# Optimization experiments

Hardware: AMD Instinct MI355X
Metric: run time of the kernel (lower is better)

Reference implementation:

```python
import jax, jax.numpy as jnp
import numpy as np
import math

B, NB, HID, KD, NH = 256, 16, 512, 64, 8

def setup_inputs() -> dict:
    key = jax.random.key(0)
    ks = jax.random.split(key, 6)
    s = lambda fan_in: 1.0 / math.sqrt(fan_in)
    return {
        "h": jax.random.normal(ks[0], (B, NB, HID), dtype=jnp.float32),
        "mask": jax.random.randint(ks[1], (B, NB), 0, 2, dtype=jnp.int32),
        "Wk": jax.random.normal(ks[2], (NB, HID, KD * NH), dtype=jnp.float32) * s(HID),
        "Wq": jax.random.normal(ks[3], (NB, HID, KD * NH), dtype=jnp.float32) * s(HID),
        "Wv": jax.random.normal(ks[4], (NB, HID, HID * NH), dtype=jnp.float32) * s(HID),
        "Wo": jax.random.normal(ks[5], (NB, HID * NH, HID), dtype=jnp.float32) * s(HID * NH),
    }

def _group_linear(x, w):
    # x: (B, NB, din), w: (NB, din, dout) -> (B, NB, dout)
    return jnp.einsum('bnd,nde->bne', x, w)

def reference(h, mask, Wk, Wq, Wv, Wo):
    # grouped QKV projections
    k = _group_linear(h, Wk).reshape(B, NB, NH, KD).transpose(0, 2, 1, 3)    # (B,H,NB,KD)
    q = _group_linear(h, Wq).reshape(B, NB, NH, KD).transpose(0, 2, 1, 3)    # (B,H,NB,KD)
    v = _group_linear(h, Wv).reshape(B, NB, NH, HID).transpose(0, 2, 1, 3)   # (B,H,NB,HID)
    scores = jnp.einsum('bhqd,bhkd->bhqk', q, k) / math.sqrt(KD)             # (B,H,NB,NB)
    probs = jax.nn.softmax(scores, axis=-1)
    # post-softmax row mask: mask (B,NB) -> (B,1,NB,1)
    probs = probs * mask.astype(probs.dtype)[:, None, :, None]
    ctx = jnp.einsum('bhqk,bhkd->bhqd', probs, v)                            # (B,H,NB,HID)
    ctx = ctx.transpose(0, 2, 1, 3).reshape(B, NB, NH * HID)                 # (B,NB,H*HID)
    return _group_linear(ctx, Wo)                                            # (B,NB,HID)
```

## Files before the change

kernel.cpp:

```cpp
#include <hip/hip_runtime.h>


typedef short s16x4 __attribute__((ext_vector_type(4)));
typedef short s16x8 __attribute__((ext_vector_type(8)));
typedef float f32x4 __attribute__((ext_vector_type(4)));

__device__ __forceinline__ unsigned short f2bf(float f) {
  unsigned int u = __builtin_bit_cast(unsigned int, f);
  u += 0x7fffu + ((u >> 16) & 1u);
  return (unsigned short)(u >> 16);
}
__device__ __forceinline__ float bf2f(unsigned short s) {
  unsigned int u = ((unsigned int)s) << 16;
  return __builtin_bit_cast(float, u);
}

__global__ __launch_bounds__(256) void cvt_h(const float* __restrict__ h,
                                             unsigned short* __restrict__ hb)
{
  int i = (blockIdx.x * 256 + threadIdx.x) * 4;
  float4 v = *reinterpret_cast<const float4*>(h + i);
  s16x4 st = { (short)f2bf(v.x), (short)f2bf(v.y), (short)f2bf(v.z), (short)f2bf(v.w) };
  *reinterpret_cast<s16x4*>(hb + i) = st;
}

__global__ __launch_bounds__(512) void qkv_gemm(
    const unsigned short* __restrict__ hb, const float* __restrict__ Wq,
    const float* __restrict__ Wk, const float* __restrict__ Wv,
    unsigned short* __restrict__ qo, unsigned short* __restrict__ ko,
    unsigned short* __restrict__ vo)
{
  const int g    = blockIdx.y;
  const int n0   = blockIdx.x * 64;
  const int tid  = threadIdx.x;
  const int lane = tid & 63;
  const int wave = tid >> 6;
  const int wm   = (wave >> 1) * 64;
  const int wn   = (wave & 1) * 32;

  const float* W; unsigned short* out; size_t obase; int oldc, wN, c0;
  if (n0 < 512)       { W = Wq + (size_t)g * 262144;  out = qo; obase = (size_t)g * 512;  oldc = 8192;  wN = 512;  c0 = n0; }
  else if (n0 < 1024) { W = Wk + (size_t)g * 262144;  out = ko; obase = (size_t)g * 512;  oldc = 8192;  wN = 512;  c0 = n0 - 512; }
  else                { W = Wv + (size_t)g * 2097152; out = vo; obase = (size_t)g * 4096; oldc = 65536; wN = 4096; c0 = n0 - 1024; }

  const unsigned short* A = hb + (size_t)g * 512;

  __shared__ unsigned short As[256][40];
  __shared__ unsigned short Bs[64][36];

  f32x4 acc[4][2];
  #pragma unroll
  for (int i = 0; i < 4; i++)
    #pragma unroll
    for (int j = 0; j < 2; j++) acc[i][j] = (f32x4){0.f, 0.f, 0.f, 0.f};

  const int fr = lane & 15, fq = lane >> 4;
  const int arow = tid >> 2, akq = tid & 3;
  const int bn = tid & 63, bkc = tid >> 6;

  s16x8 aR0[2], aR1[2];
  f32x4 bR0, bR1;

  auto LOAD0 = [&](int k0) {
    #pragma unroll
    for (int p = 0; p < 2; p++)
      aR0[p] = *reinterpret_cast<const s16x8*>(A + (size_t)(p * 128 + arow) * 8192 + k0 + akq * 8);
    const float* wp = W + (size_t)(k0 + bkc * 4) * wN + c0 + bn;
    bR0 = (f32x4){ wp[0], wp[wN], wp[2 * wN], wp[3 * wN] };
  };
  auto LOAD1 = [&](int k0) {
    #pragma unroll
    for (int p = 0; p < 2; p++)
      aR1[p] = *reinterpret_cast<const s16x8*>(A + (size_t)(p * 128 + arow) * 8192 + k0 + akq * 8);
    const float* wp = W + (size_t)(k0 + bkc * 4) * wN + c0 + bn;
    bR1 = (f32x4){ wp[0], wp[wN], wp[2 * wN], wp[3 * wN] };
  };
  auto STORE0 = [&]() {
    #pragma unroll
    for (int p = 0; p < 2; p++)
      *reinterpret_cast<s16x8*>(&As[p * 128 + arow][akq * 8]) = aR0[p];
    s16x4 st = { (short)f2bf(bR0[0]), (short)f2bf(bR0[1]),
                 (short)f2bf(bR0[2]), (short)f2bf(bR0[3]) };
    *reinterpret_cast<s16x4*>(&Bs[bn][bkc * 4]) = st;
  };
  auto STORE1 = [&]() {
    #pragma unroll
    for (int p = 0; p < 2; p++)
      *reinterpret_cast<s16x8*>(&As[p * 128 + arow][akq * 8]) = aR1[p];
    s16x4 st = { (short)f2bf(bR1[0]), (short)f2bf(bR1[1]),
                 (short)f2bf(bR1[2]), (short)f2bf(bR1[3]) };
    *reinterpret_cast<s16x4*>(&Bs[bn][bkc * 4]) = st;
  };
  auto COMPUTE = [&]() {
    s16x8 af[4], bfr[2];
    #pragma unroll
    for (int mi = 0; mi < 4; mi++)
      af[mi] = *reinterpret_cast<const s16x8*>(&As[wm + mi * 16 + fr][fq * 8]);
    #pragma unroll
    for (int ni = 0; ni < 2; ni++) {
      const s16x4* bp = reinterpret_cast<const s16x4*>(&Bs[wn + ni * 16 + fr][fq * 8]);
      s16x4 lo = bp[0], hi = bp[1];
      bfr[ni] = __builtin_shufflevector(lo, hi, 0, 1, 2, 3, 4, 5, 6, 7);
    }
    #pragma unroll
    for (int mi = 0; mi < 4; mi++)
      #pragma unroll
      for (int ni = 0; ni < 2; ni++)
        acc[mi][ni] = __builtin_amdgcn_mfma_f32_16x16x32_bf16(af[mi], bfr[ni], acc[mi][ni], 0, 0, 0);
  };

  LOAD0(0);
  LOAD1(32);
  STORE0();
  __syncthreads();

  for (int k0 = 0; k0 < 512; k0 += 64) {
    if (k0 + 64 < 512) LOAD0(k0 + 64);
    COMPUTE();
    __syncthreads();
    STORE1();
    __syncthreads();
    if (k0 + 96 < 512) LOAD1(k0 + 96);
    COMPUTE();
    if (k0 + 64 < 512) {
      __syncthreads();
      STORE0();
      __syncthreads();
    }
  }

  #pragma unroll
  for (int mi = 0; mi < 4; mi++)
    #pragma unroll
    for (int ni = 0; ni < 2; ni++)
      #pragma unroll
      for (int r = 0; r < 4; r++) {
        int row = wm + mi * 16 + fq * 4 + r;
        int col = c0 + wn + ni * 16 + fr;
        out[obase + (size_t)row * oldc + col] = f2bf(acc[mi][ni][r]);
      }
}

__global__ __launch_bounds__(256) void attn_kernel(
    const unsigned short* __restrict__ q, const unsigned short* __restrict__ k,
    const unsigned short* __restrict__ v, const int* __restrict__ mask,
    unsigned short* __restrict__ ctx)
{
  const int b  = blockIdx.x >> 3;
  const int hh = blockIdx.x & 7;
  const int tid = threadIdx.x;

  __shared__ float qs[16][65];
  __shared__ float ks[16][65];
  __shared__ float sc[16][16];

  {
    int n = tid >> 4, d4 = (tid & 15) * 4;
    size_t gi = ((size_t)(b * 16 + n) << 9) + (hh << 6) + d4;
    ushort4 qv = *reinterpret_cast<const ushort4*>(q + gi);
    ushort4 kv = *reinterpret_cast<const ushort4*>(k + gi);
    qs[n][d4] = bf2f(qv.x); qs[n][d4+1] = bf2f(qv.y); qs[n][d4+2] = bf2f(qv.z); qs[n][d4+3] = bf2f(qv.w);
    ks[n][d4] = bf2f(kv.x); ks[n][d4+1] = bf2f(kv.y); ks[n][d4+2] = bf2f(kv.z); ks[n][d4+3] = bf2f(kv.w);
  }
  __syncthreads();
  {
    int qi = tid >> 4, ki = tid & 15;
    float s = 0.f;
    #pragma unroll
    for (int j = 0; j < 64; j++) s += qs[qi][j] * ks[ki][j];
    sc[qi][ki] = s * 0.125f;
  }
  __syncthreads();
  if (tid < 16) {
    float m = sc[tid][0];
    #pragma unroll
    for (int j = 1; j < 16; j++) m = fmaxf(m, sc[tid][j]);
    float ev[16], sum = 0.f;
    #pragma unroll
    for (int j = 0; j < 16; j++) { ev[j] = __expf(sc[tid][j] - m); sum += ev[j]; }
    float scale = (mask[b * 16 + tid] != 0) ? (1.f / sum) : 0.f;
    #pragma unroll
    for (int j = 0; j < 16; j++) sc[tid][j] = ev[j] * scale;
  }
  __syncthreads();
  {
    int col4  = (tid & 127) * 4;
    int qbase = (tid >> 7) * 8;
    float a0[8], a1[8], a2[8], a3[8];
    #pragma unroll
    for (int j = 0; j < 8; j++) { a0[j] = 0.f; a1[j] = 0.f; a2[j] = 0.f; a3[j] = 0.f; }
    #pragma unroll
    for (int kk = 0; kk < 16; kk++) {
      ushort4 vv = *reinterpret_cast<const ushort4*>(
          v + ((size_t)(b * 16 + kk) << 12) + (hh << 9) + col4);
      float v0 = bf2f(vv.x), v1 = bf2f(vv.y), v2 = bf2f(vv.z), v3 = bf2f(vv.w);
      #pragma unroll
      for (int j = 0; j < 8; j++) {
        float p = sc[qbase + j][kk];
        a0[j] += p * v0; a1[j] += p * v1; a2[j] += p * v2; a3[j] += p * v3;
      }
    }
    #pragma unroll
    for (int j = 0; j < 8; j++) {
      ushort4 st = { f2bf(a0[j]), f2bf(a1[j]), f2bf(a2[j]), f2bf(a3[j]) };
      *reinterpret_cast<ushort4*>(
          ctx + ((size_t)(b * 16 + qbase + j) << 12) + (hh << 9) + col4) = st;
    }
  }
}

__global__ __launch_bounds__(512) void out_gemm(
    const unsigned short* __restrict__ ctxp, const float* __restrict__ Wo,
    float* __restrict__ partial)
{
  const int g    = blockIdx.y;
  const int bx   = blockIdx.x;
  const int sk   = bx >> 3;
  const int n0   = (bx & 7) * 64;
  const int tid  = threadIdx.x;
  const int lane = tid & 63;
  const int wave = tid >> 6;
  const int wm   = (wave >> 1) * 64;
  const int wn   = (wave & 1) * 32;

  const unsigned short* A = ctxp + (size_t)g * 4096;
  const float* W = Wo + (size_t)g * 2097152;

  __shared__ unsigned short As[256][40];
  __shared__ unsigned short Bs[64][36];

  f32x4 acc[4][2];
  #pragma unroll
  for (int i = 0; i < 4; i++)
    #pragma unroll
    for (int j = 0; j < 2; j++) acc[i][j] = (f32x4){0.f, 0.f, 0.f, 0.f};

  const int fr = lane & 15, fq = lane >> 4;
  const int arow = tid >> 2, akq = tid & 3;
  const int bn = tid & 63, bkc = tid >> 6;

  s16x8 aR0[2], aR1[2];
  f32x4 bR0, bR1;

  auto LOAD0 = [&](int k0) {
    #pragma unroll
    for (int p = 0; p < 2; p++)
      aR0[p] = *reinterpret_cast<const s16x8*>(A + (size_t)(p * 128 + arow) * 65536 + k0 + akq * 8);
    const float* wp = W + (size_t)(k0 + bkc * 4) * 512 + n0 + bn;
    bR0 = (f32x4){ wp[0], wp[512], wp[1024], wp[1536] };
  };
  auto LOAD1 = [&](int k0) {
    #pragma unroll
    for (int p = 0; p < 2; p++)
      aR1[p] = *reinterpret_cast<const s16x8*>(A + (size_t)(p * 128 + arow) * 65536 + k0 + akq * 8);
    const float* wp = W + (size_t)(k0 + bkc * 4) * 512 + n0 + bn;
    bR1 = (f32x4){ wp[0], wp[512], wp[1024], wp[1536] };
  };
  auto STORE0 = [&]() {
    #pragma unroll
    for (int p = 0; p < 2; p++)
      *reinterpret_cast<s16x8*>(&As[p * 128 + arow][akq * 8]) = aR0[p];
    s16x4 st = { (short)f2bf(bR0[0]), (short)f2bf(bR0[1]),
                 (short)f2bf(bR0[2]), (short)f2bf(bR0[3]) };
    *reinterpret_cast<s16x4*>(&Bs[bn][bkc * 4]) = st;
  };
  auto STORE1 = [&]() {
    #pragma unroll
    for (int p = 0; p < 2; p++)
      *reinterpret_cast<s16x8*>(&As[p * 128 + arow][akq * 8]) = aR1[p];
    s16x4 st = { (short)f2bf(bR1[0]), (short)f2bf(bR1[1]),
                 (short)f2bf(bR1[2]), (short)f2bf(bR1[3]) };
    *reinterpret_cast<s16x4*>(&Bs[bn][bkc * 4]) = st;
  };
  auto COMPUTE = [&]() {
    s16x8 af[4], bfr[2];
    #pragma unroll
    for (int mi = 0; mi < 4; mi++)
      af[mi] = *reinterpret_cast<const s16x8*>(&As[wm + mi * 16 + fr][fq * 8]);
    #pragma unroll
    for (int ni = 0; ni < 2; ni++) {
      const s16x4* bp = reinterpret_cast<const s16x4*>(&Bs[wn + ni * 16 + fr][fq * 8]);
      s16x4 lo = bp[0], hi = bp[1];
      bfr[ni] = __builtin_shufflevector(lo, hi, 0, 1, 2, 3, 4, 5, 6, 7);
    }
    #pragma unroll
    for (int mi = 0; mi < 4; mi++)
      #pragma unroll
      for (int ni = 0; ni < 2; ni++)
        acc[mi][ni] = __builtin_amdgcn_mfma_f32_16x16x32_bf16(af[mi], bfr[ni], acc[mi][ni], 0, 0, 0);
  };

  const int ks = sk * 1024, kend = ks + 1024;

  LOAD0(ks);
  LOAD1(ks + 32);
  STORE0();
  __syncthreads();

  for (int k0 = ks; k0 < kend; k0 += 64) {
    if (k0 + 64 < kend) LOAD0(k0 + 64);
    COMPUTE();
    __syncthreads();
    STORE1();
    __syncthreads();
    if (k0 + 96 < kend) LOAD1(k0 + 96);
    COMPUTE();
    if (k0 + 64 < kend) {
      __syncthreads();
      STORE0();
      __syncthreads();
    }
  }

  float* pg = partial + (size_t)sk * 2097152 + (size_t)g * 512;
  #pragma unroll
  for (int mi = 0; mi < 4; mi++)
    #pragma unroll
    for (int ni = 0; ni < 2; ni++)
      #pragma unroll
      for (int r = 0; r < 4; r++) {
        int row = wm + mi * 16 + fq * 4 + r;
        int col = n0 + wn + ni * 16 + fr;
        pg[(size_t)row * 8192 + col] = acc[mi][ni][r];
      }
}

__global__ __launch_bounds__(256) void reduce4(const float* __restrict__ part,
                                               float* __restrict__ out)
{
  int i = (blockIdx.x * 256 + threadIdx.x) * 4;
  float4 a = *reinterpret_cast<const float4*>(part + i);
  float4 b = *reinterpret_cast<const float4*>(part + 2097152 + i);
  float4 c = *reinterpret_cast<const float4*>(part + 4194304 + i);
  float4 d = *reinterpret_cast<const float4*>(part + 6291456 + i);
  float4 s = { a.x + b.x + c.x + d.x, a.y + b.y + c.y + d.y,
               a.z + b.z + c.z + d.z, a.w + b.w + c.w + d.w };
  *reinterpret_cast<float4*>(out + i) = s;
}

extern "C" void kernel_launch(void* const* d_in, const int* in_sizes, int n_in,
                              void* d_out, int out_size, void* d_ws, size_t ws_size,
                              hipStream_t stream) {
  const float* h  = (const float*)d_in[0];
  const int* mask = (const int*)d_in[1];
  const float* Wk = (const float*)d_in[2];
  const float* Wq = (const float*)d_in[3];
  const float* Wv = (const float*)d_in[4];
  const float* Wo = (const float*)d_in[5];
  float* out = (float*)d_out;

  unsigned short* qws   = (unsigned short*)d_ws;
  unsigned short* kws   = qws + 2097152;
  unsigned short* vws   = kws + 2097152;
  unsigned short* ctxws = vws + 16777216;
  unsigned short* hb    = ctxws;
  float* part           = (float*)d_ws;

  cvt_h<<<2048, 256, 0, stream>>>(h, hb);
  qkv_gemm<<<dim3(80, 16), 512, 0, stream>>>(hb, Wq, Wk, Wv, qws, kws, vws);
  attn_kernel<<<2048, 256, 0, stream>>>(qws, kws, vws, mask, ctxws);
  out_gemm<<<dim3(32, 16), 512, 0, stream>>>(ctxws, Wo, part);
  reduce4<<<2048, 256, 0, stream>>>(part, out);
}
```

Before: 389.8 us.

## Double-buffer LDS tiles in GEMMs to halve barriers per k-step

Both the QKV and output GEMMs now keep two LDS buffers, one per half-step, so each store goes to the buffer not being read. This removes one of the two block barriers around each store. The plain __syncthreads is replaced by an explicit lgkmcnt wait plus s_barrier, and the B-weight global loads are issued before the A loads. LDS use per block doubles, which may lower occupancy. The lighter barrier may not order the global loads the way __syncthreads did.

```diff
diff --git a/kernel.cpp b/kernel.cpp
--- a/kernel.cpp
+++ b/kernel.cpp
@@ -13,6 +13,11 @@
 __device__ __forceinline__ float bf2f(unsigned short s) {
   unsigned int u = ((unsigned int)s) << 16;
   return __builtin_bit_cast(float, u);
+}
+
+__device__ __forceinline__ void lds_barrier() {
+  asm volatile("s_waitcnt lgkmcnt(0)" ::: "memory");
+  __builtin_amdgcn_s_barrier();
 }
 
 __global__ __launch_bounds__(256) void cvt_h(const float* __restrict__ h,
@@ -45,8 +50,8 @@
 
   const unsigned short* A = hb + (size_t)g * 512;
 
-  __shared__ unsigned short As[256][40];
-  __shared__ unsigned short Bs[64][36];
+  __shared__ unsigned short As[2][256][40];
+  __shared__ unsigned short Bs[2][64][36];
 
   f32x4 acc[4][2];
   #pragma unroll
@@ -62,43 +67,43 @@
   f32x4 bR0, bR1;
 
   auto LOAD0 = [&](int k0) {
-    #pragma unroll
-    for (int p = 0; p < 2; p++)
-      aR0[p] = *reinterpret_cast<const s16x8*>(A + (size_t)(p * 128 + arow) * 8192 + k0 + akq * 8);
     const float* wp = W + (size_t)(k0 + bkc * 4) * wN + c0 + bn;
     bR0 = (f32x4){ wp[0], wp[wN], wp[2 * wN], wp[3 * wN] };
+    #pragma unroll
+    for (int p = 0; p < 2; p++)
+      aR0[p] = *reinterpret_cast<const s16x8*>(A + (size_t)(p * 128 + arow) * 8192 + k0 + akq * 8);
   };
   auto LOAD1 = [&](int k0) {
-    #pragma unroll
-    for (int p = 0; p < 2; p++)
-      aR1[p] = *reinterpret_cast<const s16x8*>(A + (size_t)(p * 128 + arow) * 8192 + k0 + akq * 8);
     const float* wp = W + (size_t)(k0 + bkc * 4) * wN + c0 + bn;
     bR1 = (f32x4){ wp[0], wp[wN], wp[2 * wN], wp[3 * wN] };
+    #pragma unroll
+    for (int p = 0; p < 2; p++)
+      aR1[p] = *reinterpret_cast<const s16x8*>(A + (size_t)(p * 128 + arow) * 8192 + k0 + akq * 8);
   };
   auto STORE0 = [&]() {
     #pragma unroll
     for (int p = 0; p < 2; p++)
-      *reinterpret_cast<s16x8*>(&As[p * 128 + arow][akq * 8]) = aR0[p];
+      *reinterpret_cast<s16x8*>(&As[0][p * 128 + arow][akq * 8]) = aR0[p];
     s16x4 st = { (short)f2bf(bR0[0]), (short)f2bf(bR0[1]),
                  (short)f2bf(bR0[2]), (short)f2bf(bR0[3]) };
-    *reinterpret_cast<s16x4*>(&Bs[bn][bkc * 4]) = st;
+    *reinterpret_cast<s16x4*>(&Bs[0][bn][bkc * 4]) = st;
   };
   auto STORE1 = [&]() {
     #pragma unroll
     for (int p = 0; p < 2; p++)
-      *reinterpret_cast<s16x8*>(&As[p * 128 + arow][akq * 8]) = aR1[p];
+      *reinterpret_cast<s16x8*>(&As[1][p * 128 + arow][akq * 8]) = aR1[p];
     s16x4 st = { (short)f2bf(bR1[0]), (short)f2bf(bR1[1]),
                  (short)f2bf(bR1[2]), (short)f2bf(bR1[3]) };
-    *reinterpret_cast<s16x4*>(&Bs[bn][bkc * 4]) = st;
-  };
-  auto COMPUTE = [&]() {
+    *reinterpret_cast<s16x4*>(&Bs[1][bn][bkc * 4]) = st;
+  };
+  auto COMPUTE = [&](int buf) {
     s16x8 af[4], bfr[2];
     #pragma unroll
     for (int mi = 0; mi < 4; mi++)
-      af[mi] = *reinterpret_cast<const s16x8*>(&As[wm + mi * 16 + fr][fq * 8]);
+      af[mi] = *reinterpret_cast<const s16x8*>(&As[buf][wm + mi * 16 + fr][fq * 8]);
     #pragma unroll
     for (int ni = 0; ni < 2; ni++) {
-      const s16x4* bp = reinterpret_cast<const s16x4*>(&Bs[wn + ni * 16 + fr][fq * 8]);
+      const s16x4* bp = reinterpret_cast<const s16x4*>(&Bs[buf][wn + ni * 16 + fr][fq * 8]);
       s16x4 lo = bp[0], hi = bp[1];
       bfr[ni] = __builtin_shufflevector(lo, hi, 0, 1, 2, 3, 4, 5, 6, 7);
     }
@@ -112,20 +117,18 @@
   LOAD0(0);
   LOAD1(32);
   STORE0();
-  __syncthreads();
+  lds_barrier();
 
   for (int k0 = 0; k0 < 512; k0 += 64) {
     if (k0 + 64 < 512) LOAD0(k0 + 64);
-    COMPUTE();
-    __syncthreads();
+    COMPUTE(0);
     STORE1();
-    __syncthreads();
+    lds_barrier();
     if (k0 + 96 < 512) LOAD1(k0 + 96);
-    COMPUTE();
+    COMPUTE(1);
     if (k0 + 64 < 512) {
-      __syncthreads();
       STORE0();
-      __syncthreads();
+      lds_barrier();
     }
   }
 
@@ -226,8 +229,8 @@
   const unsigned short* A = ctxp + (size_t)g * 4096;
   const float* W = Wo + (size_t)g * 2097152;
 
-  __shared__ unsigned short As[256][40];
-  __shared__ unsigned short Bs[64][36];
+  __shared__ unsigned short As[2][256][40];
+  __shared__ unsigned short Bs[2][64][36];
 
   f32x4 acc[4][2];
   #pragma unroll
@@ -243,43 +246,43 @@
   f32x4 bR0, bR1;
 
   auto LOAD0 = [&](int k0) {
-    #pragma unroll
-    for (int p = 0; p < 2; p++)
-      aR0[p] = *reinterpret_cast<const s16x8*>(A + (size_t)(p * 128 + arow) * 65536 + k0 + akq * 8);
     const float* wp = W + (size_t)(k0 + bkc * 4) * 512 + n0 + bn;
     bR0 = (f32x4){ wp[0], wp[512], wp[1024], wp[1536] };
+    #pragma unroll
+    for (int p = 0; p < 2; p++)
+      aR0[p] = *reinterpret_cast<const s16x8*>(A + (size_t)(p * 128 + arow) * 65536 + k0 + akq * 8);
   };
   auto LOAD1 = [&](int k0) {
-    #pragma unroll
-    for (int p = 0; p < 2; p++)
-      aR1[p] = *reinterpret_cast<const s16x8*>(A + (size_t)(p * 128 + arow) * 65536 + k0 + akq * 8);
     const float* wp = W + (size_t)(k0 + bkc * 4) * 512 + n0 + bn;
     bR1 = (f32x4){ wp[0], wp[512], wp[1024], wp[1536] };
+    #pragma unroll
+    for (int p = 0; p < 2; p++)
+      aR1[p] = *reinterpret_cast<const s16x8*>(A + (size_t)(p * 128 + arow) * 65536 + k0 + akq * 8);
   };
   auto STORE0 = [&]() {
     #pragma unroll
     for (int p = 0; p < 2; p++)
-      *reinterpret_cast<s16x8*>(&As[p * 128 + arow][akq * 8]) = aR0[p];
+      *reinterpret_cast<s16x8*>(&As[0][p * 128 + arow][akq * 8]) = aR0[p];
     s16x4 st = { (short)f2bf(bR0[0]), (short)f2bf(bR0[1]),
                  (short)f2bf(bR0[2]), (short)f2bf(bR0[3]) };
-    *reinterpret_cast<s16x4*>(&Bs[bn][bkc * 4]) = st;
+    *reinterpret_cast<s16x4*>(&Bs[0][bn][bkc * 4]) = st;
   };
   auto STORE1 = [&]() {
     #pragma unroll
     for (int p = 0; p < 2; p++)
-      *reinterpret_cast<s16x8*>(&As[p * 128 + arow][akq * 8]) = aR1[p];
+      *reinterpret_cast<s16x8*>(&As[1][p * 128 + arow][akq * 8]) = aR1[p];
     s16x4 st = { (short)f2bf(bR1[0]), (short)f2bf(bR1[1]),
                  (short)f2bf(bR1[2]), (short)f2bf(bR1[3]) };
-    *reinterpret_cast<s16x4*>(&Bs[bn][bkc * 4]) = st;
-  };
-  auto COMPUTE = [&]() {
+    *reinterpret_cast<s16x4*>(&Bs[1][bn][bkc * 4]) = st;
+  };
+  auto COMPUTE = [&](int buf) {
     s16x8 af[4], bfr[2];
     #pragma unroll
     for (int mi = 0; mi < 4; mi++)
-      af[mi] = *reinterpret_cast<const s16x8*>(&As[wm + mi * 16 + fr][fq * 8]);
+      af[mi] = *reinterpret_cast<const s16x8*>(&As[buf][wm + mi * 16 + fr][fq * 8]);
     #pragma unroll
     for (int ni = 0; ni < 2; ni++) {
-      const s16x4* bp = reinterpret_cast<const s16x4*>(&Bs[wn + ni * 16 + fr][fq * 8]);
+      const s16x4* bp = reinterpret_cast<const s16x4*>(&Bs[buf][wn + ni * 16 + fr][fq * 8]);
       s16x4 lo = bp[0], hi = bp[1];
       bfr[ni] = __builtin_shufflevector(lo, hi, 0, 1, 2, 3, 4, 5, 6, 7);
     }
@@ -295,20 +298,18 @@
   LOAD0(ks);
   LOAD1(ks + 32);
   STORE0();
-  __syncthreads();
+  lds_barrier();
 
   for (int k0 = ks; k0 < kend; k0 += 64) {
     if (k0 + 64 < kend) LOAD0(k0 + 64);
-    COMPUTE();
-    __syncthreads();
+    COMPUTE(0);
     STORE1();
-    __syncthreads();
+    lds_barrier();
     if (k0 + 96 < kend) LOAD1(k0 + 96);
-    COMPUTE();
+    COMPUTE(1);
     if (k0 + 64 < kend) {
-      __syncthreads();
       STORE0();
-      __syncthreads();
+      lds_barrier();
     }
   }
 
```

New measurement: 392.1 us. About the same (+0.6%).
